# Performance work log

Hardware: AMD Instinct MI355X
Metric: run time of the kernel (lower is better)

## Reference

```python
import jax, jax.numpy as jnp
import numpy as np

N_EMBD = 1024
BLOCK_SIZE = 128
HEAD_SIZE = 128
THETA = 10000.0


def setup_inputs() -> dict:
    key = jax.random.key(0)
    k1, k2, k3, k4 = jax.random.split(key, 4)
    B, T = 256, BLOCK_SIZE
    x = jax.random.normal(k1, (B, T, N_EMBD), dtype=jnp.float32)
    # nn.Linear(n_embd, head_size, bias=False) stored as [n_embd, head_size] so y = x @ W
    s = 1.0 / np.sqrt(N_EMBD)
    Wq = jax.random.normal(k2, (N_EMBD, HEAD_SIZE), dtype=jnp.float32) * s
    Wk = jax.random.normal(k3, (N_EMBD, HEAD_SIZE), dtype=jnp.float32) * s
    Wv = jax.random.normal(k4, (N_EMBD, HEAD_SIZE), dtype=jnp.float32) * s
    return {"x": x, "Wq": Wq, "Wk": Wk, "Wv": Wv}


def _rope_cos_sin(T: int, head_size: int):
    # freqs = exp(arange(0, hs, 2) * (-log(theta)/hs)); angles = outer(t, freqs)
    inv_freq = jnp.exp(jnp.arange(0, head_size, 2, dtype=jnp.float32) * (-np.log(THETA) / head_size))
    angles = jnp.arange(T, dtype=jnp.float32)[:, None] * inv_freq[None, :]  # [T, hs/2]
    return jnp.cos(angles), jnp.sin(angles)


def _apply_rope(t, cos, sin):
    # complex-view rotation on interleaved (even, odd) pairs of the last dim
    tr = t[..., 0::2]  # real parts  [B,T,hs/2]
    ti = t[..., 1::2]  # imag parts
    out_r = tr * cos - ti * sin
    out_i = tr * sin + ti * cos
    return jnp.stack([out_r, out_i], axis=-1).reshape(t.shape)


def reference(x, Wq, Wk, Wv):
    B, T, _ = x.shape
    hs = Wq.shape[1]
    q = x @ Wq  # [B,T,hs]
    k = x @ Wk
    v = x @ Wv
    cos, sin = _rope_cos_sin(T, hs)
    q = _apply_rope(q, cos, sin)
    k = _apply_rope(k, cos, sin)
    scores = jnp.einsum('btd,bsd->bts', q, k) / jnp.sqrt(jnp.asarray(hs, q.dtype))
    causal = jnp.tril(jnp.ones((T, T), dtype=bool))
    scores = jnp.where(causal[None, :, :], scores, -jnp.inf)
    att = jax.nn.softmax(scores, axis=-1)  # dropout is identity in eval
    return jnp.einsum('bts,bsd->btd', att, v)
```

## Files before the change

### kernel.cpp

```cpp
#include <hip/hip_runtime.h>
#include <math.h>

typedef __bf16 bf16x8 __attribute__((ext_vector_type(8)));
typedef float  f32x4  __attribute__((ext_vector_type(4)));
typedef unsigned short us4 __attribute__((ext_vector_type(4)));

constexpr int N_EMBD = 1024;
constexpr int T_SEQ  = 128;
constexpr int HS     = 128;
constexpr int BATCH  = 256;
constexpr int ROWS   = BATCH * T_SEQ;

__device__ __forceinline__ void async16(const void* g, void* l) {
    __builtin_amdgcn_global_load_lds(
        (const __attribute__((address_space(1))) unsigned int*)g,
        (__attribute__((address_space(3))) unsigned int*)l, 16, 0, 0);
}
__device__ __forceinline__ unsigned short bfbits(float f) {
    return __builtin_bit_cast(unsigned short, (__bf16)f);
}
__device__ __forceinline__ f32x4 zero4() {
    f32x4 z = {0.f, 0.f, 0.f, 0.f};
    return z;
}

__global__ __launch_bounds__(256) void wcast(
    const float* __restrict__ Wq, const float* __restrict__ Wk,
    const float* __restrict__ Wv, unsigned short* __restrict__ Wt)
{
    __shared__ unsigned short tile[64][130];
    const int bid = blockIdx.x;
    const int nt  = bid >> 4;
    const int k0  = (bid & 15) << 6;
    const float* src = (nt == 0) ? Wq : ((nt == 1) ? Wk : Wv);
    const int tid = threadIdx.x;
#pragma unroll
    for (int j = 0; j < 32; ++j) {
        int idx = tid + j * 256;
        int k = idx >> 7, n = idx & 127;
        tile[k][n] = bfbits(src[(size_t)(k0 + k) * HS + n]);
    }
    __syncthreads();
#pragma unroll
    for (int j = 0; j < 32; ++j) {
        int idx = tid + j * 256;
        int n = idx >> 6, kk = idx & 63;
        Wt[(size_t)(nt * 128 + n) * N_EMBD + k0 + kk] = tile[kk][n];
    }
}

__global__ __launch_bounds__(256) void qkv_gemm(
    const float* __restrict__ x,
    const unsigned short* __restrict__ Wt,
    unsigned short* __restrict__ qb,
    unsigned short* __restrict__ kb,
    unsigned short* __restrict__ vt)
{
    __shared__ char lds[49152];
    const int tid = threadIdx.x;
    const int w  = tid >> 6;
    const int l  = tid & 63;
    const int cl = l & 15;
    const int quad = l >> 4;
    const int nt  = blockIdx.x >> 8;
    const int mt  = blockIdx.x & 255;
    const int row0 = mt << 7;
    const int wm0 = (w & 1) << 6;
    const int wn0 = (w >> 1) << 6;

    f32x4 acc[4][4];
#pragma unroll
    for (int a = 0; a < 4; ++a)
#pragma unroll
        for (int b = 0; b < 4; ++b) acc[a][b] = zero4();

    for (int kc = 0; kc < N_EMBD; kc += 64) {
        __syncthreads();
#pragma unroll
        for (int jj = 0; jj < 8; ++jj) {
            int j = w * 8 + jj;
            int m = j * 4 + (l >> 4);
            int csrc = (l & 15) ^ (m & 15);
            async16(x + (size_t)(row0 + m) * N_EMBD + kc + csrc * 4, lds + j * 1024);
        }
#pragma unroll
        for (int jj = 0; jj < 4; ++jj) {
            int j = w * 4 + jj;
            int n = j * 8 + (l >> 3);
            int csrc = (l & 7) ^ (l >> 3);
            async16(Wt + (size_t)(nt * 128 + n) * N_EMBD + kc + csrc * 8,
                    lds + 32768 + j * 1024);
        }
        __syncthreads();

#pragma unroll
        for (int ks = 0; ks < 2; ++ks) {
            const int kq = ks * 4 + quad;
            bf16x8 af[4], bf[4];
#pragma unroll
            for (int rt = 0; rt < 4; ++rt) {
                int m = wm0 + rt * 16 + cl;
                int c0 = kq * 2;
                f32x4 a0 = *(const f32x4*)(lds + ((m * 16 + (c0 ^ cl)) << 4));
                f32x4 a1 = *(const f32x4*)(lds + ((m * 16 + ((c0 + 1) ^ cl)) << 4));
                bf16x8 t;
                t[0] = (__bf16)a0[0]; t[1] = (__bf16)a0[1];
                t[2] = (__bf16)a0[2]; t[3] = (__bf16)a0[3];
                t[4] = (__bf16)a1[0]; t[5] = (__bf16)a1[1];
                t[6] = (__bf16)a1[2]; t[7] = (__bf16)a1[3];
                af[rt] = t;
            }
#pragma unroll
            for (int ct = 0; ct < 4; ++ct) {
                int n = wn0 + ct * 16 + cl;
                bf[ct] = *(const bf16x8*)(lds + 32768 + ((n * 8 + (kq ^ (l & 7))) << 4));
            }
#pragma unroll
            for (int rt = 0; rt < 4; ++rt)
#pragma unroll
                for (int ct = 0; ct < 4; ++ct)
                    acc[rt][ct] = __builtin_amdgcn_mfma_f32_16x16x32_bf16(
                        af[rt], bf[ct], acc[rt][ct], 0, 0, 0);
        }
    }

    if (nt < 2) {
        unsigned short* dst = (nt == 0) ? qb : kb;
        const float LNT = 0.07195578430905272f;
#pragma unroll
        for (int ct = 0; ct < 4; ++ct) {
            int c = wn0 + ct * 16 + cl;
            float freq = __expf(-(float)(c & ~1) * LNT);
#pragma unroll
            for (int rt = 0; rt < 4; ++rt) {
#pragma unroll
                for (int i = 0; i < 4; ++i) {
                    int t = wm0 + rt * 16 + quad * 4 + i;
                    float v = acc[rt][ct][i];
                    float p = __shfl_xor(v, 1);
                    float sn, cs;
                    __sincosf((float)t * freq, &sn, &cs);
                    float r = ((c & 1) == 0) ? (v * cs - p * sn) : (p * sn + v * cs);
                    dst[(size_t)(row0 + t) * HS + c] = bfbits(r);
                }
            }
        }
    } else {
#pragma unroll
        for (int ct = 0; ct < 4; ++ct) {
            int d = wn0 + ct * 16 + cl;
#pragma unroll
            for (int rt = 0; rt < 4; ++rt) {
                int s0 = wm0 + rt * 16 + quad * 4;
                us4 u;
                u.x = bfbits(acc[rt][ct][0]);
                u.y = bfbits(acc[rt][ct][1]);
                u.z = bfbits(acc[rt][ct][2]);
                u.w = bfbits(acc[rt][ct][3]);
                *(us4*)(vt + (size_t)mt * 16384 + d * 128 + s0) = u;
            }
        }
    }
}

__global__ __launch_bounds__(64) void attn(
    const unsigned short* __restrict__ qb,
    const unsigned short* __restrict__ kb,
    const unsigned short* __restrict__ vt,
    float* __restrict__ out)
{
    __shared__ char plds[32 * 272];
    const int l = threadIdx.x;
    const int cl = l & 15;
    const int quad = l >> 4;
    const int b  = blockIdx.x >> 2;
    const int rg = blockIdx.x & 3;
    const int nct = rg * 2 + 2;

    const unsigned short* qB = qb + (size_t)b * 16384;
    const unsigned short* kB = kb + (size_t)b * 16384;
    const unsigned short* vB = vt + (size_t)b * 16384;

    f32x4 s[2][8];
#pragma unroll
    for (int rt = 0; rt < 2; ++rt)
#pragma unroll
        for (int ct = 0; ct < 8; ++ct) s[rt][ct] = zero4();

#pragma unroll 1
    for (int ks = 0; ks < 4; ++ks) {
        int kq = ks * 4 + quad;
        bf16x8 a0 = *(const bf16x8*)(qB + (size_t)(rg * 32 + cl) * HS + kq * 8);
        bf16x8 a1 = *(const bf16x8*)(qB + (size_t)(rg * 32 + 16 + cl) * HS + kq * 8);
#pragma unroll
        for (int ct = 0; ct < 8; ++ct) {
            if (ct < nct) {
                bf16x8 bb = *(const bf16x8*)(kB + (size_t)(ct * 16 + cl) * HS + kq * 8);
                s[0][ct] = __builtin_amdgcn_mfma_f32_16x16x32_bf16(a0, bb, s[0][ct], 0, 0, 0);
                s[1][ct] = __builtin_amdgcn_mfma_f32_16x16x32_bf16(a1, bb, s[1][ct], 0, 0, 0);
            }
        }
    }

    const float scale = 0.08838834764831845f;
#pragma unroll
    for (int rt = 0; rt < 2; ++rt) {
#pragma unroll
        for (int i = 0; i < 4; ++i) {
            int t = rg * 32 + rt * 16 + quad * 4 + i;
            float mx = -3.0e38f;
#pragma unroll
            for (int ct = 0; ct < 8; ++ct) if (ct < nct) {
                int col = ct * 16 + cl;
                float v = s[rt][ct][i] * scale;
                v = (col <= t) ? v : -INFINITY;
                s[rt][ct][i] = v;
                mx = fmaxf(mx, v);
            }
            mx = fmaxf(mx, __shfl_xor(mx, 1));
            mx = fmaxf(mx, __shfl_xor(mx, 2));
            mx = fmaxf(mx, __shfl_xor(mx, 4));
            mx = fmaxf(mx, __shfl_xor(mx, 8));
            float sum = 0.f;
#pragma unroll
            for (int ct = 0; ct < 8; ++ct) if (ct < nct) {
                float p = __expf(s[rt][ct][i] - mx);
                s[rt][ct][i] = p;
                sum += p;
            }
            sum += __shfl_xor(sum, 1);
            sum += __shfl_xor(sum, 2);
            sum += __shfl_xor(sum, 4);
            sum += __shfl_xor(sum, 8);
            float inv = 1.0f / sum;
            int rl = rt * 16 + quad * 4 + i;
#pragma unroll
            for (int ct = 0; ct < 8; ++ct) if (ct < nct) {
                *(unsigned short*)(plds + rl * 272 + (ct * 16 + cl) * 2) =
                    bfbits(s[rt][ct][i] * inv);
            }
        }
    }

    f32x4 o[2][8];
#pragma unroll
    for (int rt = 0; rt < 2; ++rt)
#pragma unroll
        for (int ct = 0; ct < 8; ++ct) o[rt][ct] = zero4();

    const int nks = rg + 1;
    for (int ks = 0; ks < nks; ++ks) {
        int kq = ks * 4 + quad;
        bf16x8 a0 = *(const bf16x8*)(plds + cl * 272 + kq * 16);
        bf16x8 a1 = *(const bf16x8*)(plds + (16 + cl) * 272 + kq * 16);
#pragma unroll
        for (int ct = 0; ct < 8; ++ct) {
            bf16x8 bb = *(const bf16x8*)(vB + (size_t)(ct * 16 + cl) * 128 + kq * 8);
            o[0][ct] = __builtin_amdgcn_mfma_f32_16x16x32_bf16(a0, bb, o[0][ct], 0, 0, 0);
            o[1][ct] = __builtin_amdgcn_mfma_f32_16x16x32_bf16(a1, bb, o[1][ct], 0, 0, 0);
        }
    }

#pragma unroll
    for (int rt = 0; rt < 2; ++rt)
#pragma unroll
        for (int ct = 0; ct < 8; ++ct)
#pragma unroll
            for (int i = 0; i < 4; ++i) {
                int t = rg * 32 + rt * 16 + quad * 4 + i;
                out[(size_t)b * 16384 + (size_t)t * HS + ct * 16 + cl] = o[rt][ct][i];
            }
}

extern "C" void kernel_launch(void* const* d_in, const int* in_sizes, int n_in,
                              void* d_out, int out_size, void* d_ws, size_t ws_size,
                              hipStream_t stream) {
    const float* x  = (const float*)d_in[0];
    const float* Wq = (const float*)d_in[1];
    const float* Wk = (const float*)d_in[2];
    const float* Wv = (const float*)d_in[3];
    float* out = (float*)d_out;

    unsigned short* qb = (unsigned short*)d_ws;
    unsigned short* kb = qb + (size_t)ROWS * HS;
    unsigned short* vt = kb + (size_t)ROWS * HS;
    unsigned short* Wt = vt + (size_t)ROWS * HS;

    wcast<<<48, 256, 0, stream>>>(Wq, Wk, Wv, Wt);
    qkv_gemm<<<768, 256, 0, stream>>>(x, Wt, qb, kb, vt);
    attn<<<1024, 64, 0, stream>>>(qb, kb, vt, out);
}
```

Baseline: 264.5 us.

## Fuse QKV into one 64x384 tile per block and split attention into 16-row blocks

The QKV GEMM now gives each 512-thread block a 64-row by 384-column tile covering Q, K and V together, instead of separate 128x128 tiles per projection. The fp32 x tile is therefore loaded from global memory once rather than three times. The attention kernel now uses 16-row query blocks (2048 blocks), which skips more of the causal work and balances load more finely, and it keeps Q fragments in registers. The costs are fewer GEMM blocks (512) each carrying more register and LDS pressure, and extra zero-padding writes to LDS for odd-sized P tiles.

```diff
diff --git a/kernel.cpp b/kernel.cpp
--- a/kernel.cpp
+++ b/kernel.cpp
@@ -49,56 +49,54 @@
     }
 }
 
-__global__ __launch_bounds__(256) void qkv_gemm(
+__global__ __launch_bounds__(512, 4) void qkv_gemm(
     const float* __restrict__ x,
     const unsigned short* __restrict__ Wt,
     unsigned short* __restrict__ qb,
     unsigned short* __restrict__ kb,
     unsigned short* __restrict__ vt)
 {
-    __shared__ char lds[49152];
+    __shared__ char lds[65536];
     const int tid = threadIdx.x;
     const int w  = tid >> 6;
     const int l  = tid & 63;
     const int cl = l & 15;
     const int quad = l >> 4;
-    const int nt  = blockIdx.x >> 8;
-    const int mt  = blockIdx.x & 255;
-    const int row0 = mt << 7;
-    const int wm0 = (w & 1) << 6;
-    const int wn0 = (w >> 1) << 6;
-
-    f32x4 acc[4][4];
-#pragma unroll
-    for (int a = 0; a < 4; ++a)
-#pragma unroll
-        for (int b = 0; b < 4; ++b) acc[a][b] = zero4();
+    const int mt  = blockIdx.x;
+    const int row0 = mt << 6;
+    const int wm0 = (w & 1) << 5;
+    const int wn0 = (w >> 1) * 96;
+
+    f32x4 acc[2][6];
+#pragma unroll
+    for (int a = 0; a < 2; ++a)
+#pragma unroll
+        for (int b = 0; b < 6; ++b) acc[a][b] = zero4();
 
     for (int kc = 0; kc < N_EMBD; kc += 64) {
         __syncthreads();
 #pragma unroll
-        for (int jj = 0; jj < 8; ++jj) {
-            int j = w * 8 + jj;
+        for (int jj = 0; jj < 2; ++jj) {
+            int j = w * 2 + jj;
             int m = j * 4 + (l >> 4);
             int csrc = (l & 15) ^ (m & 15);
             async16(x + (size_t)(row0 + m) * N_EMBD + kc + csrc * 4, lds + j * 1024);
         }
 #pragma unroll
-        for (int jj = 0; jj < 4; ++jj) {
-            int j = w * 4 + jj;
+        for (int jj = 0; jj < 6; ++jj) {
+            int j = w * 6 + jj;
             int n = j * 8 + (l >> 3);
             int csrc = (l & 7) ^ (l >> 3);
-            async16(Wt + (size_t)(nt * 128 + n) * N_EMBD + kc + csrc * 8,
-                    lds + 32768 + j * 1024);
+            async16(Wt + (size_t)n * N_EMBD + kc + csrc * 8, lds + 16384 + j * 1024);
         }
         __syncthreads();
 
 #pragma unroll
         for (int ks = 0; ks < 2; ++ks) {
             const int kq = ks * 4 + quad;
-            bf16x8 af[4], bf[4];
-#pragma unroll
-            for (int rt = 0; rt < 4; ++rt) {
+            bf16x8 af[2], bf[6];
+#pragma unroll
+            for (int rt = 0; rt < 2; ++rt) {
                 int m = wm0 + rt * 16 + cl;
                 int c0 = kq * 2;
                 f32x4 a0 = *(const f32x4*)(lds + ((m * 16 + (c0 ^ cl)) << 4));
@@ -111,53 +109,54 @@
                 af[rt] = t;
             }
 #pragma unroll
-            for (int ct = 0; ct < 4; ++ct) {
+            for (int ct = 0; ct < 6; ++ct) {
                 int n = wn0 + ct * 16 + cl;
-                bf[ct] = *(const bf16x8*)(lds + 32768 + ((n * 8 + (kq ^ (l & 7))) << 4));
-            }
-#pragma unroll
-            for (int rt = 0; rt < 4; ++rt)
-#pragma unroll
-                for (int ct = 0; ct < 4; ++ct)
+                bf[ct] = *(const bf16x8*)(lds + 16384 + ((n * 8 + (kq ^ (l & 7))) << 4));
+            }
+#pragma unroll
+            for (int rt = 0; rt < 2; ++rt)
+#pragma unroll
+                for (int ct = 0; ct < 6; ++ct)
                     acc[rt][ct] = __builtin_amdgcn_mfma_f32_16x16x32_bf16(
                         af[rt], bf[ct], acc[rt][ct], 0, 0, 0);
         }
     }
 
-    if (nt < 2) {
-        unsigned short* dst = (nt == 0) ? qb : kb;
-        const float LNT = 0.07195578430905272f;
-#pragma unroll
-        for (int ct = 0; ct < 4; ++ct) {
-            int c = wn0 + ct * 16 + cl;
-            float freq = __expf(-(float)(c & ~1) * LNT);
-#pragma unroll
-            for (int rt = 0; rt < 4; ++rt) {
+    const float LNT = 0.07195578430905272f;
+    const int bidx = row0 >> 7;
+    const int srow0 = row0 & 127;
+#pragma unroll
+    for (int ct = 0; ct < 6; ++ct) {
+        int c  = wn0 + ct * 16 + cl;
+        int ntc = c >> 7;
+        int d  = c & 127;
+        if (ntc < 2) {
+            unsigned short* dst = (ntc == 0) ? qb : kb;
+            float freq = __expf(-(float)(d & ~1) * LNT);
+#pragma unroll
+            for (int rt = 0; rt < 2; ++rt) {
 #pragma unroll
                 for (int i = 0; i < 4; ++i) {
-                    int t = wm0 + rt * 16 + quad * 4 + i;
+                    int grow = row0 + wm0 + rt * 16 + quad * 4 + i;
+                    int t = grow & 127;
                     float v = acc[rt][ct][i];
                     float p = __shfl_xor(v, 1);
                     float sn, cs;
                     __sincosf((float)t * freq, &sn, &cs);
-                    float r = ((c & 1) == 0) ? (v * cs - p * sn) : (p * sn + v * cs);
-                    dst[(size_t)(row0 + t) * HS + c] = bfbits(r);
+                    float r = ((d & 1) == 0) ? (v * cs - p * sn) : (p * sn + v * cs);
+                    dst[(size_t)grow * HS + d] = bfbits(r);
                 }
             }
-        }
-    } else {
-#pragma unroll
-        for (int ct = 0; ct < 4; ++ct) {
-            int d = wn0 + ct * 16 + cl;
-#pragma unroll
-            for (int rt = 0; rt < 4; ++rt) {
-                int s0 = wm0 + rt * 16 + quad * 4;
+        } else {
+#pragma unroll
+            for (int rt = 0; rt < 2; ++rt) {
+                int s0 = srow0 + wm0 + rt * 16 + quad * 4;
                 us4 u;
                 u.x = bfbits(acc[rt][ct][0]);
                 u.y = bfbits(acc[rt][ct][1]);
                 u.z = bfbits(acc[rt][ct][2]);
                 u.w = bfbits(acc[rt][ct][3]);
-                *(us4*)(vt + (size_t)mt * 16384 + d * 128 + s0) = u;
+                *(us4*)(vt + (size_t)bidx * 16384 + d * 128 + s0) = u;
             }
         }
     }
@@ -169,107 +168,106 @@
     const unsigned short* __restrict__ vt,
     float* __restrict__ out)
 {
-    __shared__ char plds[32 * 272];
+    __shared__ char plds[16 * 272];
     const int l = threadIdx.x;
     const int cl = l & 15;
     const int quad = l >> 4;
-    const int b  = blockIdx.x >> 2;
-    const int rg = blockIdx.x & 3;
-    const int nct = rg * 2 + 2;
+    const int b  = blockIdx.x >> 3;
+    const int rg = blockIdx.x & 7;
+    const int nct = rg + 1;
+    const int nks = (rg + 2) >> 1;
 
     const unsigned short* qB = qb + (size_t)b * 16384;
     const unsigned short* kB = kb + (size_t)b * 16384;
     const unsigned short* vB = vt + (size_t)b * 16384;
 
-    f32x4 s[2][8];
-#pragma unroll
-    for (int rt = 0; rt < 2; ++rt)
-#pragma unroll
-        for (int ct = 0; ct < 8; ++ct) s[rt][ct] = zero4();
-
-#pragma unroll 1
-    for (int ks = 0; ks < 4; ++ks) {
-        int kq = ks * 4 + quad;
-        bf16x8 a0 = *(const bf16x8*)(qB + (size_t)(rg * 32 + cl) * HS + kq * 8);
-        bf16x8 a1 = *(const bf16x8*)(qB + (size_t)(rg * 32 + 16 + cl) * HS + kq * 8);
-#pragma unroll
-        for (int ct = 0; ct < 8; ++ct) {
-            if (ct < nct) {
-                bf16x8 bb = *(const bf16x8*)(kB + (size_t)(ct * 16 + cl) * HS + kq * 8);
-                s[0][ct] = __builtin_amdgcn_mfma_f32_16x16x32_bf16(a0, bb, s[0][ct], 0, 0, 0);
-                s[1][ct] = __builtin_amdgcn_mfma_f32_16x16x32_bf16(a1, bb, s[1][ct], 0, 0, 0);
-            }
+    bf16x8 af[4];
+#pragma unroll
+    for (int ks = 0; ks < 4; ++ks)
+        af[ks] = *(const bf16x8*)(qB + (size_t)(rg * 16 + cl) * HS + (ks * 4 + quad) * 8);
+
+    f32x4 s[8];
+#pragma unroll
+    for (int ct = 0; ct < 8; ++ct) s[ct] = zero4();
+
+#pragma unroll
+    for (int ct = 0; ct < 8; ++ct) if (ct < nct) {
+        const unsigned short* kr = kB + (size_t)(ct * 16 + cl) * HS;
+#pragma unroll
+        for (int ks = 0; ks < 4; ++ks) {
+            bf16x8 bb = *(const bf16x8*)(kr + (ks * 4 + quad) * 8);
+            s[ct] = __builtin_amdgcn_mfma_f32_16x16x32_bf16(af[ks], bb, s[ct], 0, 0, 0);
         }
     }
 
     const float scale = 0.08838834764831845f;
 #pragma unroll
-    for (int rt = 0; rt < 2; ++rt) {
+    for (int i = 0; i < 4; ++i) {
+        int t = rg * 16 + quad * 4 + i;
+        float mx = -3.0e38f;
+#pragma unroll
+        for (int ct = 0; ct < 8; ++ct) if (ct < nct) {
+            int col = ct * 16 + cl;
+            float v = s[ct][i] * scale;
+            v = (col <= t) ? v : -INFINITY;
+            s[ct][i] = v;
+            mx = fmaxf(mx, v);
+        }
+        mx = fmaxf(mx, __shfl_xor(mx, 1));
+        mx = fmaxf(mx, __shfl_xor(mx, 2));
+        mx = fmaxf(mx, __shfl_xor(mx, 4));
+        mx = fmaxf(mx, __shfl_xor(mx, 8));
+        float sum = 0.f;
+#pragma unroll
+        for (int ct = 0; ct < 8; ++ct) if (ct < nct) {
+            float p = __expf(s[ct][i] - mx);
+            s[ct][i] = p;
+            sum += p;
+        }
+        sum += __shfl_xor(sum, 1);
+        sum += __shfl_xor(sum, 2);
+        sum += __shfl_xor(sum, 4);
+        sum += __shfl_xor(sum, 8);
+        float inv = 1.0f / sum;
+        int rl = quad * 4 + i;
+#pragma unroll
+        for (int ct = 0; ct < 8; ++ct) if (ct < nct) {
+            *(unsigned short*)(plds + rl * 272 + (ct * 16 + cl) * 2) =
+                bfbits(s[ct][i] * inv);
+        }
+    }
+    if ((rg & 1) == 0) {
+#pragma unroll
+        for (int i = 0; i < 4; ++i)
+            *(unsigned short*)(plds + (quad * 4 + i) * 272 + (nct * 16 + cl) * 2) = 0;
+    }
+
+    bf16x8 ap[4];
+#pragma unroll
+    for (int ks = 0; ks < 4; ++ks) if (ks < nks)
+        ap[ks] = *(const bf16x8*)(plds + cl * 272 + (ks * 4 + quad) * 16);
+
+    f32x4 o[8];
+#pragma unroll
+    for (int ct = 0; ct < 8; ++ct) o[ct] = zero4();
+
+#pragma unroll
+    for (int ct = 0; ct < 8; ++ct) {
+        const unsigned short* vr = vB + (size_t)(ct * 16 + cl) * 128;
+#pragma unroll
+        for (int ks = 0; ks < 4; ++ks) if (ks < nks) {
+            bf16x8 bb = *(const bf16x8*)(vr + (ks * 4 + quad) * 8);
+            o[ct] = __builtin_amdgcn_mfma_f32_16x16x32_bf16(ap[ks], bb, o[ct], 0, 0, 0);
+        }
+    }
+
+#pragma unroll
+    for (int ct = 0; ct < 8; ++ct)
 #pragma unroll
         for (int i = 0; i < 4; ++i) {
-            int t = rg * 32 + rt * 16 + quad * 4 + i;
-            float mx = -3.0e38f;
-#pragma unroll
-            for (int ct = 0; ct < 8; ++ct) if (ct < nct) {
-                int col = ct * 16 + cl;
-                float v = s[rt][ct][i] * scale;
-                v = (col <= t) ? v : -INFINITY;
-                s[rt][ct][i] = v;
-                mx = fmaxf(mx, v);
-            }
-            mx = fmaxf(mx, __shfl_xor(mx, 1));
-            mx = fmaxf(mx, __shfl_xor(mx, 2));
-            mx = fmaxf(mx, __shfl_xor(mx, 4));
-            mx = fmaxf(mx, __shfl_xor(mx, 8));
-            float sum = 0.f;
-#pragma unroll
-            for (int ct = 0; ct < 8; ++ct) if (ct < nct) {
-                float p = __expf(s[rt][ct][i] - mx);
-                s[rt][ct][i] = p;
-                sum += p;
-            }
-            sum += __shfl_xor(sum, 1);
-            sum += __shfl_xor(sum, 2);
-            sum += __shfl_xor(sum, 4);
-            sum += __shfl_xor(sum, 8);
-            float inv = 1.0f / sum;
-            int rl = rt * 16 + quad * 4 + i;
-#pragma unroll
-            for (int ct = 0; ct < 8; ++ct) if (ct < nct) {
-                *(unsigned short*)(plds + rl * 272 + (ct * 16 + cl) * 2) =
-                    bfbits(s[rt][ct][i] * inv);
-            }
-        }
-    }
-
-    f32x4 o[2][8];
-#pragma unroll
-    for (int rt = 0; rt < 2; ++rt)
-#pragma unroll
-        for (int ct = 0; ct < 8; ++ct) o[rt][ct] = zero4();
-
-    const int nks = rg + 1;
-    for (int ks = 0; ks < nks; ++ks) {
-        int kq = ks * 4 + quad;
-        bf16x8 a0 = *(const bf16x8*)(plds + cl * 272 + kq * 16);
-        bf16x8 a1 = *(const bf16x8*)(plds + (16 + cl) * 272 + kq * 16);
-#pragma unroll
-        for (int ct = 0; ct < 8; ++ct) {
-            bf16x8 bb = *(const bf16x8*)(vB + (size_t)(ct * 16 + cl) * 128 + kq * 8);
-            o[0][ct] = __builtin_amdgcn_mfma_f32_16x16x32_bf16(a0, bb, o[0][ct], 0, 0, 0);
-            o[1][ct] = __builtin_amdgcn_mfma_f32_16x16x32_bf16(a1, bb, o[1][ct], 0, 0, 0);
-        }
-    }
-
-#pragma unroll
-    for (int rt = 0; rt < 2; ++rt)
-#pragma unroll
-        for (int ct = 0; ct < 8; ++ct)
-#pragma unroll
-            for (int i = 0; i < 4; ++i) {
-                int t = rg * 32 + rt * 16 + quad * 4 + i;
-                out[(size_t)b * 16384 + (size_t)t * HS + ct * 16 + cl] = o[rt][ct][i];
-            }
+            int t = rg * 16 + quad * 4 + i;
+            out[(size_t)b * 16384 + (size_t)t * HS + ct * 16 + cl] = o[ct][i];
+        }
 }
 
 extern "C" void kernel_launch(void* const* d_in, const int* in_sizes, int n_in,
@@ -287,6 +285,6 @@
     unsigned short* Wt = vt + (size_t)ROWS * HS;
 
     wcast<<<48, 256, 0, stream>>>(Wq, Wk, Wv, Wt);
-    qkv_gemm<<<768, 256, 0, stream>>>(x, Wt, qb, kb, vt);
-    attn<<<1024, 64, 0, stream>>>(qb, kb, vt, out);
-}
+    qkv_gemm<<<512, 512, 0, stream>>>(x, Wt, qb, kb, vt);
+    attn<<<2048, 64, 0, stream>>>(qb, kb, vt, out);
+}
```

Result: faster. 250.4 us (-5.3%).
